# Performance work log

Measured on AMD Instinct MI355X. Metric: run time of the kernel, lower is better.

Reference implementation:

```python
import jax, jax.numpy as jnp
import numpy as np

N = 100000
E = 3200000


def setup_inputs() -> dict:
    key = jax.random.key(0)
    ks = jax.random.split(key, 8)
    x = jax.random.normal(ks[0], (N,), dtype=jnp.float32)
    edge_index = jax.random.randint(ks[1], (2, E), 0, N, dtype=jnp.int32)
    W_in = jax.random.normal(ks[2], (1, 32), dtype=jnp.float32) * 0.5
    b_in = jnp.zeros((32,), dtype=jnp.float32)
    W_mid = jax.random.normal(ks[3], (32, 32), dtype=jnp.float32) * (1.0 / np.sqrt(32))
    b_mid = jnp.zeros((32,), dtype=jnp.float32)
    W_out = jax.random.normal(ks[4], (32, 1), dtype=jnp.float32) * (1.0 / np.sqrt(32))
    b_out = jnp.zeros((1,), dtype=jnp.float32)
    return {"x": x, "edge_index": edge_index, "W_in": W_in, "b_in": b_in,
            "W_mid": W_mid, "b_mid": b_mid, "W_out": W_out, "b_out": b_out}


def _gcn_layer(h, src, dst, norm, W, b, n_nodes):
    # linear transform first (out_dim <= in_dim keeps message traffic small)
    h = h @ W                              # [N, out]
    msg = h[src] * norm[:, None]           # gather + edge-normalize, [E+N, out]
    out = jax.ops.segment_sum(msg, dst, num_segments=n_nodes)  # scatter-add
    return out + b


def reference(x, edge_index, W_in, b_in, W_mid, b_mid, W_out, b_out):
    n = x.shape[0]
    # add_self_loops
    loops = jnp.arange(n, dtype=edge_index.dtype)
    src = jnp.concatenate([edge_index[0], loops])
    dst = jnp.concatenate([edge_index[1], loops])
    # symmetric degree normalization (GCN): deg over target nodes incl. self loops
    deg = jax.ops.segment_sum(jnp.ones_like(src, dtype=x.dtype), dst, num_segments=n)
    dinv = jnp.where(deg > 0, jax.lax.rsqrt(deg), 0.0)
    norm = dinv[src] * dinv[dst]           # [E+N]

    h = x[:, None]                         # view(-1, 1)
    h = jax.nn.relu(_gcn_layer(h, src, dst, norm, W_in, b_in, n))
    h = jax.nn.relu(_gcn_layer(h, src, dst, norm, W_mid, b_mid, n))
    h = jax.nn.relu(_gcn_layer(h, src, dst, norm, W_mid, b_mid, n))  # conv_mid reused (shared weights)
    h = _gcn_layer(h, src, dst, norm, W_out, b_out, n)
    return jax.nn.sigmoid(h)               # [N, 1]
```

## Files before the change

### kernel.cpp

```cpp
#include <hip/hip_runtime.h>
#include <math.h>


#define BLK 256
#define PBLK 1024
#define BBLK 512
#define NBLK 256
#define MAXCHUNK 12544
#define BCAP 5120
#define SCAP 8448
#define SZCLAMP 5120

#define FP8_SCALE 64.0f
#define FP8_INV   0.015625f

typedef float f32x2 __attribute__((ext_vector_type(2)));


__global__ void k_initcur(int* __restrict__ cursor, int NB,
                          int* __restrict__ ph1, int* __restrict__ ph2) {
    int b = blockIdx.x * blockDim.x + threadIdx.x;
    if (b < NB) cursor[b] = b * BCAP;
    if (b < 8) { ph1[b] = 0; ph2[b] = 0; }
}

__global__ void __launch_bounds__(PBLK) k_place(
        const int* __restrict__ src, const int* __restrict__ dst,
        int* __restrict__ cursor, int* __restrict__ bkt, int E, int chunk) {
    __shared__ int hist[788];
    __shared__ int lofs[788];
    __shared__ int lcur[788];
    __shared__ int tmp[PBLK];
    __shared__ int stage[MAXCHUNK];
    int t = threadIdx.x;
    int b0 = blockIdx.x * chunk;
    int b1 = min(E, b0 + chunk);
    int n = b1 - b0;
    if (t < 788) hist[t] = 0;
    __syncthreads();
    for (int k = b0 + t; k < b1; k += PBLK) atomicAdd(&hist[dst[k] >> 7], 1);
    __syncthreads();
    int v = (t < 788) ? hist[t] : 0;
    tmp[t] = v;
    __syncthreads();
    for (int o = 1; o < PBLK; o <<= 1) {
        int a = (t >= o) ? tmp[t - o] : 0;
        __syncthreads();
        tmp[t] += a;
        __syncthreads();
    }
    int ex = tmp[t] - v;
    if (t < 788) { lofs[t] = ex; lcur[t] = ex; }
    __syncthreads();
    if (t < 782) {
        int c = hist[t];
        hist[t] = c ? atomicAdd(&cursor[t], c) : 0;
    }
    __syncthreads();
    for (int k = b0 + t; k < b1; k += PBLK) {
        int d = dst[k], s = src[k];
        int b = d >> 7;
        int p = atomicAdd(&lcur[b], 1);
        stage[p] = s | ((d & 127) << 17);
    }
    __syncthreads();
    for (int k = t; k < n; k += PBLK) {
        int lo = 0, hi = 781;
        while (lo < hi) {
            int mid = (lo + hi + 1) >> 1;
            if (lofs[mid] <= k) lo = mid; else hi = mid - 1;
        }
        int pos = hist[lo] + (k - lofs[lo]);
        if (pos < (lo + 1) * BCAP) bkt[pos] = stage[k];
    }
}

__global__ void __launch_bounds__(BBLK) k_build(
        const int* __restrict__ cursor, const int* __restrict__ bkt,
        const float* __restrict__ x,
        uint2* __restrict__ rs2, int* __restrict__ ss,
        float* __restrict__ dinv, float* __restrict__ sa, int N) {
    __shared__ int cnt[1024], lofs[1024], lcur[1024];
    __shared__ int tmp[BBLK];
    __shared__ int stg[SCAP];
    __shared__ int pB[128], pL[128];
    int b = blockIdx.x, t = threadIdx.x;
    int node_base = b << 7;
    int gb = b * BCAP;
    int gbs = b * SCAP;
    int sz = min(cursor[b] - gb, SZCLAMP);
    for (int i = t; i < 1024; i += BBLK) cnt[i] = 0;
    __syncthreads();
    const int* q = bkt + gb;
    for (int k = t; k < sz; k += BBLK) {
        int v = q[k];
        int bin = (((v >> 17) & 127) << 3) | ((v & 0x1FFFF) >> 14);
        atomicAdd(&cnt[bin], 1);
    }
    __syncthreads();
    int vals[2];
    int sum = 0;
    int i0 = t << 1;
    #pragma unroll
    for (int r = 0; r < 2; ++r) { vals[r] = cnt[i0 + r]; sum += vals[r]; }
    tmp[t] = sum;
    __syncthreads();
    for (int o = 1; o < BBLK; o <<= 1) {
        int a = (t >= o) ? tmp[t - o] : 0;
        __syncthreads();
        tmp[t] += a;
        __syncthreads();
    }
    int run = tmp[t] - sum;
    #pragma unroll
    for (int r = 0; r < 2; ++r) {
        int c = vals[r];
        lofs[i0 + r] = run;
        lcur[i0 + r] = run;
        run += c;
    }
    __syncthreads();
    int len = 0, padl = 0, real = 0;
    if (t < 128) {
        int i = node_base + t;
        if (i < N) {
            real = 1;
            int beg = lofs[t << 3];
            int end = (t < 127) ? lofs[(t + 1) << 3] : sz;
            len = end - beg;
            int deg = len + 1;
            padl = (deg + 7) & ~7;
            if (padl < 64) padl = 64;
        }
    }
    tmp[t] = (t < 128) ? padl : 0;
    __syncthreads();
    for (int o = 1; o < 128; o <<= 1) {
        int a = (t >= o && t < 128) ? tmp[t - o] : 0;
        __syncthreads();
        if (t < 128) tmp[t] += a;
        __syncthreads();
    }
    if (t < 128) {
        int pbeg = tmp[t] - padl;
        pB[t] = pbeg;
        pL[t] = real ? len : -1;
        if (real) {
            int i = node_base + t;
            int deg = len + 1;
            rs2[i] = make_uint2((unsigned)(gbs + pbeg), (unsigned)deg);
            float d = rsqrtf((float)deg);
            dinv[i] = d;
            sa[i] = x[i] * d;
        }
    }
    __syncthreads();
    int szp = min(tmp[127], SCAP);
    for (int i = t; i < 1024; i += BBLK) {
        int nn = i >> 3;
        lcur[i] = pB[nn] + (lofs[i] - lofs[nn << 3]);
    }
    __syncthreads();
    for (int k = t; k < sz; k += BBLK) {
        int v = q[k];
        int bin = (((v >> 17) & 127) << 3) | ((v & 0x1FFFF) >> 14);
        int pos = atomicAdd(&lcur[bin], 1);
        if (pos < SCAP) stg[pos] = (v & 0x1FFFF) << 5;
    }
    __syncthreads();
    if (t < 128 && pL[t] >= 0) {
        int pbeg = pB[t];
        int l2 = pL[t];
        int i = node_base + t;
        int deg = l2 + 1;
        int p2 = (deg + 7) & ~7;
        if (p2 < 64) p2 = 64;
        if (pbeg + l2 < SCAP) stg[pbeg + l2] = i << 5;
        for (int k = deg; k < p2; ++k)
            if (pbeg + k < SCAP) stg[pbeg + k] = N << 5;
    }
    __syncthreads();
    for (int k = t; k < szp; k += BBLK) ss[gbs + k] = stg[k];
}


__global__ void __launch_bounds__(BLK) k_l1aggG(
        const uint2* __restrict__ rs2, const int* __restrict__ ss,
        const float* __restrict__ sa, const float* __restrict__ dinv,
        const float* __restrict__ Win, const float* __restrict__ bin,
        const float* __restrict__ Wmid, unsigned char* __restrict__ Gh, int N) {
    __shared__ float sW[1024];
    int tid = threadIdx.x;
    #pragma unroll
    for (int r = 0; r < 4; ++r) sW[r * 256 + tid] = Wmid[r * 256 + tid];
    __syncthreads();
    int t = blockIdx.x * blockDim.x + tid;
    int i = t >> 5, l = t & 31;
    if (i >= N) return;
    uint2 r = rs2[i];
    int beg = (int)r.x, end = (int)(r.x + r.y);
    float s = 0.f;
    for (int e = beg + l; e < end; e += 32) s += sa[(unsigned)ss[e] >> 5];
    #pragma unroll
    for (int m = 16; m; m >>= 1) s += __shfl_xor(s, m, 32);
    float d = dinv[i];
    float h = d * s;
    float F = h * Win[l] + bin[l];
    F = F > 0.f ? F : 0.f;
    float g = 0.f;
    #pragma unroll
    for (int k = 0; k < 32; ++k) g += __shfl(F, k, 32) * sW[k * 32 + l];
    float v = g * d * FP8_SCALE;
    Gh[t] = (unsigned char)(__builtin_amdgcn_cvt_pk_fp8_f32(v, v, 0, false) & 0xFF);
}

__device__ __forceinline__ void acc_row(f32x2* a2, uint2 v) {
    a2[0] += __builtin_amdgcn_cvt_pk_f32_fp8(v.x, false);
    a2[1] += __builtin_amdgcn_cvt_pk_f32_fp8(v.x, true);
    a2[2] += __builtin_amdgcn_cvt_pk_f32_fp8(v.y, false);
    a2[3] += __builtin_amdgcn_cvt_pk_f32_fp8(v.y, true);
}

__device__ __forceinline__ void gather64(const unsigned char* __restrict__ Gb,
                                         const int* __restrict__ ss,
                                         int beg, int sub, int fo, int deg,
                                         f32x2* a2) {
    int sbeg = beg + sub;
    int idx[8];
    #pragma unroll
    for (int rr = 0; rr < 8; ++rr) idx[rr] = ss[sbeg + 8 * rr];
    uint2 v[8];
    #pragma unroll
    for (int rr = 0; rr < 8; ++rr)
        v[rr] = *(const uint2*)(Gb + (unsigned)(idx[rr] | fo));
    #pragma unroll
    for (int rr = 0; rr < 8; ++rr) acc_row(a2, v[rr]);
    int plen = (deg + 7) & ~7;
    plen = max(plen, 64);
    int wpl = max(plen, __shfl_xor(plen, 32));
    if (wpl > 64) {
        for (int so = 64 + sub; so < plen; so += 8) {
            int ix = ss[beg + so];
            uint2 vv = *(const uint2*)(Gb + (unsigned)(ix | fo));
            acc_row(a2, vv);
        }
    }
}

__device__ __forceinline__ void reduce_subs(f32x2* a2) {
    #pragma unroll
    for (int j = 0; j < 4; ++j) {
        #pragma unroll
        for (int m = 4; m <= 16; m <<= 1) {
            f32x2 o;
            o.x = __shfl_xor(a2[j].x, m);
            o.y = __shfl_xor(a2[j].y, m);
            a2[j] += o;
        }
    }
}

__global__ void __launch_bounds__(256) k_agg2mv(
        const uint2* __restrict__ rs2, const int* __restrict__ ss,
        const unsigned char* __restrict__ Gb, const float* __restrict__ dinv,
        const float* __restrict__ b, const float* __restrict__ Wmid,
        unsigned char* __restrict__ Gh3, int N) {
    __shared__ float sW2[1024];
    __shared__ float sF[8][34];
    __shared__ float sdv[8];
    int t = threadIdx.x;
    #pragma unroll
    for (int r = 0; r < 4; ++r) {
        int t4 = r * 256 + t;
        int k = t4 >> 5, ln = t4 & 31;
        sW2[(k >> 1) * 64 + ln * 2 + (k & 1)] = Wmid[t4];
    }
    int tg = blockIdx.x * blockDim.x + t;
    int g = tg >> 5;
    int lane = t & 31, sub = lane >> 2, fl = lane & 3;
    int grp = t >> 5;
    int fo = fl << 3;
    f32x2 a2[4];
    #pragma unroll
    for (int j = 0; j < 4; ++j) a2[j] = (f32x2)0.f;
    uint2 r = rs2[g];
    gather64(Gb, ss, (int)r.x, sub, fo, (int)r.y, a2);
    reduce_subs(a2);
    if (sub == 0) {
        float d = dinv[g];
        if (fl == 0) sdv[grp] = d;
        float ds = d * FP8_INV;
        #pragma unroll
        for (int j = 0; j < 8; ++j) {
            float v = ds * a2[j >> 1][j & 1] + b[fl * 8 + j];
            sF[grp][fl * 8 + j] = v > 0.f ? v : 0.f;
        }
    }
    __syncthreads();
    f32x2 s2 = (f32x2)0.f;
    #pragma unroll
    for (int k2 = 0; k2 < 16; ++k2) {
        f32x2 w2 = *(const f32x2*)&sW2[k2 * 64 + lane * 2];
        f32x2 f2 = *(const f32x2*)&sF[grp][k2 * 2];
        s2 += f2 * w2;
    }
    float s = s2.x + s2.y;
    float v = s * sdv[grp] * FP8_SCALE;
    Gh3[(long long)g * 32 + lane] =
        (unsigned char)(__builtin_amdgcn_cvt_pk_fp8_f32(v, v, 0, false) & 0xFF);
}

__global__ void __launch_bounds__(256) k_agg3(
        const uint2* __restrict__ rs2, const int* __restrict__ ss,
        const unsigned char* __restrict__ Gb, const float* __restrict__ dinv,
        const float* __restrict__ b, const float* __restrict__ Wout,
        float* __restrict__ sa, int N) {
    int t = blockIdx.x * blockDim.x + threadIdx.x;
    int g = t >> 5;
    if (g >= N) return;
    int lane = t & 31, sub = lane >> 2, fl = lane & 3;
    int fo = fl << 3;
    uint2 r = rs2[g];
    f32x2 a2[4];
    #pragma unroll
    for (int j = 0; j < 4; ++j) a2[j] = (f32x2)0.f;
    gather64(Gb, ss, (int)r.x, sub, fo, (int)r.y, a2);
    reduce_subs(a2);
    if (sub == 0) {
        float d = dinv[g];
        float ds = d * FP8_INV;
        float p = 0.f;
        #pragma unroll
        for (int j = 0; j < 8; ++j) {
            float v = ds * a2[j >> 1][j & 1] + b[fl * 8 + j];
            v = v > 0.f ? v : 0.f;
            p += v * Wout[fl * 8 + j];
        }
        p += __shfl_xor(p, 1, 32);
        p += __shfl_xor(p, 2, 32);
        if (fl == 0) sa[g] = p * d;
    }
}

__global__ void k_final_agg(const uint2* __restrict__ rs2, const int* __restrict__ ss,
                            const float* __restrict__ sa, const float* __restrict__ dinv,
                            const float* __restrict__ bout, float* __restrict__ out, int N) {
    int t = blockIdx.x * blockDim.x + threadIdx.x;
    int i = t >> 5, l = t & 31;
    if (i >= N) return;
    uint2 r = rs2[i];
    int beg = (int)r.x, end = (int)(r.x + r.y);
    float s = 0.f;
    for (int e = beg + l; e < end; e += 32) s += sa[(unsigned)ss[e] >> 5];
    #pragma unroll
    for (int m = 16; m; m >>= 1) s += __shfl_xor(s, m, 32);
    if (l == 0) {
        float z = dinv[i] * s + bout[0];
        out[i] = 1.0f / (1.0f + expf(-z));
    }
}

extern "C" void kernel_launch(void* const* d_in, const int* in_sizes, int n_in,
                              void* d_out, int out_size, void* d_ws, size_t ws_size,
                              hipStream_t stream) {
    const float* x    = (const float*)d_in[0];
    const int*   ei   = (const int*)  d_in[1];
    const float* Win  = (const float*)d_in[2];
    const float* bin  = (const float*)d_in[3];
    const float* Wmid = (const float*)d_in[4];
    const float* bmid = (const float*)d_in[5];
    const float* Wout = (const float*)d_in[6];
    const float* bout = (const float*)d_in[7];
    float* out = (float*)d_out;

    int N = in_sizes[0];
    int E = in_sizes[1] / 2;
    const int* src = ei;
    const int* dst = ei + E;

    int NB = (N + 127) >> 7;
    int chunk = (E + NBLK - 1) / NBLK;

    int* cursor = (int*)d_ws;
    uint2* rs2  = (uint2*)(cursor + 1024);
    int* ss     = (int*)(rs2 + N + 8);
    float* dinv = (float*)(ss + (size_t)NB * SCAP + 64);
    float* sa   = dinv + N;
    unsigned char* Gh  = (unsigned char*)(sa + N);
    unsigned char* Gh3 = Gh + 32 * (size_t)N + 32;
    int* bkt    = (int*)(Gh3 + 32 * (size_t)N + 32);

    int NT   = N * 32;
    int gN32 = (NT + BLK - 1) / BLK;

    k_initcur<<<(NB + BLK - 1) / BLK, BLK, 0, stream>>>(
        cursor, NB, (int*)(Gh + 32 * (size_t)N), (int*)(Gh3 + 32 * (size_t)N));
    k_place<<<NBLK, PBLK, 0, stream>>>(src, dst, cursor, bkt, E, chunk);
    k_build<<<NB, BBLK, 0, stream>>>(cursor, bkt, x, rs2, ss, dinv, sa, N);

    k_l1aggG<<<gN32, BLK, 0, stream>>>(rs2, ss, sa, dinv, Win, bin, Wmid, Gh, N);

    k_agg2mv<<<gN32, BLK, 0, stream>>>(rs2, ss, Gh, dinv, bmid, Wmid, Gh3, N);

    k_agg3<<<gN32, BLK, 0, stream>>>(rs2, ss, Gh3, dinv, bmid, Wout, sa, N);

    k_final_agg<<<gN32, BLK, 0, stream>>>(rs2, ss, sa, dinv, bout, out, N);
}
```

Measured before the change: 247.9 us.

## Process two nodes per wavefront-half in gather kernels and shrink per-node padding

Removes the minimum 64-slot padding per node in the CSR build, so the padded index list shrinks to degree rounded up to 8, and lowers the staging capacity to match. The layer-2 and layer-3 aggregation kernels now handle two destination nodes per 32-lane group, masking rows beyond each node's padded length to a phantom zero row. This gives more independent loads in flight per thread and halves the grid size. Layer 1's matvec is also rewritten to go through shared memory with paired float2 weights instead of 32 shuffles. The tradeoff is higher register pressure, and the smaller staging buffer could overflow for dense buckets.

```diff
diff --git a/kernel.cpp b/kernel.cpp
--- a/kernel.cpp
+++ b/kernel.cpp
@@ -8,7 +8,7 @@
 #define NBLK 256
 #define MAXCHUNK 12544
 #define BCAP 5120
-#define SCAP 8448
+#define SCAP 6144
 #define SZCLAMP 5120
 
 #define FP8_SCALE 64.0f
@@ -128,9 +128,7 @@
             int beg = lofs[t << 3];
             int end = (t < 127) ? lofs[(t + 1) << 3] : sz;
             len = end - beg;
-            int deg = len + 1;
-            padl = (deg + 7) & ~7;
-            if (padl < 64) padl = 64;
+            padl = (len + 8) & ~7;
         }
     }
     tmp[t] = (t < 128) ? padl : 0;
@@ -172,11 +170,9 @@
         int pbeg = pB[t];
         int l2 = pL[t];
         int i = node_base + t;
-        int deg = l2 + 1;
-        int p2 = (deg + 7) & ~7;
-        if (p2 < 64) p2 = 64;
+        int p2 = (l2 + 8) & ~7;
         if (pbeg + l2 < SCAP) stg[pbeg + l2] = i << 5;
-        for (int k = deg; k < p2; ++k)
+        for (int k = l2 + 1; k < p2; ++k)
             if (pbeg + k < SCAP) stg[pbeg + k] = N << 5;
     }
     __syncthreads();
@@ -189,29 +185,45 @@
         const float* __restrict__ sa, const float* __restrict__ dinv,
         const float* __restrict__ Win, const float* __restrict__ bin,
         const float* __restrict__ Wmid, unsigned char* __restrict__ Gh, int N) {
-    __shared__ float sW[1024];
+    __shared__ float sW2[1024];
+    __shared__ float sF[8][34];
     int tid = threadIdx.x;
     #pragma unroll
-    for (int r = 0; r < 4; ++r) sW[r * 256 + tid] = Wmid[r * 256 + tid];
+    for (int r = 0; r < 4; ++r) {
+        int t4 = r * 256 + tid;
+        int k = t4 >> 5, ln = t4 & 31;
+        sW2[(k >> 1) * 64 + ln * 2 + (k & 1)] = Wmid[t4];
+    }
     __syncthreads();
     int t = blockIdx.x * blockDim.x + tid;
     int i = t >> 5, l = t & 31;
-    if (i >= N) return;
-    uint2 r = rs2[i];
-    int beg = (int)r.x, end = (int)(r.x + r.y);
-    float s = 0.f;
-    for (int e = beg + l; e < end; e += 32) s += sa[(unsigned)ss[e] >> 5];
-    #pragma unroll
-    for (int m = 16; m; m >>= 1) s += __shfl_xor(s, m, 32);
-    float d = dinv[i];
-    float h = d * s;
-    float F = h * Win[l] + bin[l];
-    F = F > 0.f ? F : 0.f;
-    float g = 0.f;
-    #pragma unroll
-    for (int k = 0; k < 32; ++k) g += __shfl(F, k, 32) * sW[k * 32 + l];
-    float v = g * d * FP8_SCALE;
-    Gh[t] = (unsigned char)(__builtin_amdgcn_cvt_pk_fp8_f32(v, v, 0, false) & 0xFF);
+    int grp = tid >> 5;
+    bool act = (i < N);
+    float F = 0.f, d = 0.f;
+    if (act) {
+        uint2 r = rs2[i];
+        int beg = (int)r.x, end = (int)(r.x + r.y);
+        float s = 0.f;
+        for (int e = beg + l; e < end; e += 32) s += sa[(unsigned)ss[e] >> 5];
+        #pragma unroll
+        for (int m = 16; m; m >>= 1) s += __shfl_xor(s, m, 32);
+        d = dinv[i];
+        F = d * s * Win[l] + bin[l];
+        F = F > 0.f ? F : 0.f;
+    }
+    sF[grp][l] = F;
+    __syncthreads();
+    if (act) {
+        f32x2 s2 = (f32x2)0.f;
+        #pragma unroll
+        for (int k2 = 0; k2 < 16; ++k2) {
+            f32x2 w2 = *(const f32x2*)&sW2[k2 * 64 + l * 2];
+            f32x2 f2 = *(const f32x2*)&sF[grp][k2 * 2];
+            s2 += f2 * w2;
+        }
+        float v = (s2.x + s2.y) * d * FP8_SCALE;
+        Gh[t] = (unsigned char)(__builtin_amdgcn_cvt_pk_fp8_f32(v, v, 0, false) & 0xFF);
+    }
 }
 
 __device__ __forceinline__ void acc_row(f32x2* a2, uint2 v) {
@@ -221,29 +233,40 @@
     a2[3] += __builtin_amdgcn_cvt_pk_f32_fp8(v.y, true);
 }
 
-__device__ __forceinline__ void gather64(const unsigned char* __restrict__ Gb,
-                                         const int* __restrict__ ss,
-                                         int beg, int sub, int fo, int deg,
-                                         f32x2* a2) {
-    int sbeg = beg + sub;
-    int idx[8];
-    #pragma unroll
-    for (int rr = 0; rr < 8; ++rr) idx[rr] = ss[sbeg + 8 * rr];
-    uint2 v[8];
-    #pragma unroll
-    for (int rr = 0; rr < 8; ++rr)
-        v[rr] = *(const uint2*)(Gb + (unsigned)(idx[rr] | fo));
-    #pragma unroll
-    for (int rr = 0; rr < 8; ++rr) acc_row(a2, v[rr]);
-    int plen = (deg + 7) & ~7;
-    plen = max(plen, 64);
-    int wpl = max(plen, __shfl_xor(plen, 32));
-    if (wpl > 64) {
-        for (int so = 64 + sub; so < plen; so += 8) {
-            int ix = ss[beg + so];
-            uint2 vv = *(const uint2*)(Gb + (unsigned)(ix | fo));
-            acc_row(a2, vv);
-        }
+__device__ __forceinline__ void gather2(const unsigned char* __restrict__ Gb,
+                                        const int* __restrict__ ss,
+                                        int begA, int plenA, int begB, int plenB,
+                                        int sub, int fo, int phantom,
+                                        f32x2* aA, f32x2* aB) {
+    int sA = begA + sub, sB = begB + sub;
+    int iA[8], iB[8];
+    #pragma unroll
+    for (int r = 0; r < 8; ++r) iA[r] = ss[sA + 8 * r];
+    #pragma unroll
+    for (int r = 0; r < 8; ++r) iB[r] = ss[sB + 8 * r];
+    #pragma unroll
+    for (int r = 0; r < 8; ++r) {
+        iA[r] = (8 * r < plenA) ? iA[r] : phantom;
+        iB[r] = (8 * r < plenB) ? iB[r] : phantom;
+    }
+    uint2 vA[8], vB[8];
+    #pragma unroll
+    for (int r = 0; r < 8; ++r)
+        vA[r] = *(const uint2*)(Gb + (unsigned)(iA[r] | fo));
+    #pragma unroll
+    for (int r = 0; r < 8; ++r)
+        vB[r] = *(const uint2*)(Gb + (unsigned)(iB[r] | fo));
+    #pragma unroll
+    for (int r = 0; r < 8; ++r) acc_row(aA, vA[r]);
+    #pragma unroll
+    for (int r = 0; r < 8; ++r) acc_row(aB, vB[r]);
+    if (plenA > 64) {
+        for (int so = 64 + sub; so < plenA; so += 8)
+            acc_row(aA, *(const uint2*)(Gb + (unsigned)(ss[begA + so] | fo)));
+    }
+    if (plenB > 64) {
+        for (int so = 64 + sub; so < plenB; so += 8)
+            acc_row(aB, *(const uint2*)(Gb + (unsigned)(ss[begB + so] | fo)));
     }
 }
 
@@ -266,8 +289,8 @@
         const float* __restrict__ b, const float* __restrict__ Wmid,
         unsigned char* __restrict__ Gh3, int N) {
     __shared__ float sW2[1024];
-    __shared__ float sF[8][34];
-    __shared__ float sdv[8];
+    __shared__ float sF[8][2][34];
+    __shared__ float sdv[8][2];
     int t = threadIdx.x;
     #pragma unroll
     for (int r = 0; r < 4; ++r) {
@@ -275,39 +298,53 @@
         int k = t4 >> 5, ln = t4 & 31;
         sW2[(k >> 1) * 64 + ln * 2 + (k & 1)] = Wmid[t4];
     }
-    int tg = blockIdx.x * blockDim.x + t;
-    int g = tg >> 5;
+    int gid = (blockIdx.x * blockDim.x + t) >> 5;
+    int gA = gid * 2, gB = gA + 1;
     int lane = t & 31, sub = lane >> 2, fl = lane & 3;
     int grp = t >> 5;
     int fo = fl << 3;
-    f32x2 a2[4];
-    #pragma unroll
-    for (int j = 0; j < 4; ++j) a2[j] = (f32x2)0.f;
-    uint2 r = rs2[g];
-    gather64(Gb, ss, (int)r.x, sub, fo, (int)r.y, a2);
-    reduce_subs(a2);
+    int phantom = N << 5;
+    bool aAct = (gA < N), bAct = (gB < N);
+    uint2 rA = aAct ? rs2[gA] : make_uint2(0u, 0u);
+    uint2 rB = bAct ? rs2[gB] : make_uint2(0u, 0u);
+    int plenA = aAct ? (((int)rA.y + 7) & ~7) : 0;
+    int plenB = bAct ? (((int)rB.y + 7) & ~7) : 0;
+    f32x2 aA[4], aB[4];
+    #pragma unroll
+    for (int j = 0; j < 4; ++j) { aA[j] = (f32x2)0.f; aB[j] = (f32x2)0.f; }
+    gather2(Gb, ss, (int)rA.x, plenA, (int)rB.x, plenB, sub, fo, phantom, aA, aB);
+    reduce_subs(aA);
+    reduce_subs(aB);
     if (sub == 0) {
-        float d = dinv[g];
-        if (fl == 0) sdv[grp] = d;
-        float ds = d * FP8_INV;
+        float dA = aAct ? dinv[gA] : 0.f;
+        float dB = bAct ? dinv[gB] : 0.f;
+        if (fl == 0) { sdv[grp][0] = dA; sdv[grp][1] = dB; }
+        float dsA = dA * FP8_INV, dsB = dB * FP8_INV;
         #pragma unroll
         for (int j = 0; j < 8; ++j) {
-            float v = ds * a2[j >> 1][j & 1] + b[fl * 8 + j];
-            sF[grp][fl * 8 + j] = v > 0.f ? v : 0.f;
-        }
-    }
-    __syncthreads();
-    f32x2 s2 = (f32x2)0.f;
-    #pragma unroll
-    for (int k2 = 0; k2 < 16; ++k2) {
-        f32x2 w2 = *(const f32x2*)&sW2[k2 * 64 + lane * 2];
-        f32x2 f2 = *(const f32x2*)&sF[grp][k2 * 2];
-        s2 += f2 * w2;
-    }
-    float s = s2.x + s2.y;
-    float v = s * sdv[grp] * FP8_SCALE;
-    Gh3[(long long)g * 32 + lane] =
-        (unsigned char)(__builtin_amdgcn_cvt_pk_fp8_f32(v, v, 0, false) & 0xFF);
+            float bj = b[fl * 8 + j];
+            float vA = dsA * aA[j >> 1][j & 1] + bj;
+            float vB = dsB * aB[j >> 1][j & 1] + bj;
+            sF[grp][0][fl * 8 + j] = vA > 0.f ? vA : 0.f;
+            sF[grp][1][fl * 8 + j] = vB > 0.f ? vB : 0.f;
+        }
+    }
+    __syncthreads();
+    #pragma unroll
+    for (int n2 = 0; n2 < 2; ++n2) {
+        f32x2 s2 = (f32x2)0.f;
+        #pragma unroll
+        for (int k2 = 0; k2 < 16; ++k2) {
+            f32x2 w2 = *(const f32x2*)&sW2[k2 * 64 + lane * 2];
+            f32x2 f2 = *(const f32x2*)&sF[grp][n2][k2 * 2];
+            s2 += f2 * w2;
+        }
+        float v = (s2.x + s2.y) * sdv[grp][n2] * FP8_SCALE;
+        int g = gA + n2;
+        if (g < N)
+            Gh3[(long long)g * 32 + lane] =
+                (unsigned char)(__builtin_amdgcn_cvt_pk_fp8_f32(v, v, 0, false) & 0xFF);
+    }
 }
 
 __global__ void __launch_bounds__(256) k_agg3(
@@ -316,29 +353,45 @@
         const float* __restrict__ b, const float* __restrict__ Wout,
         float* __restrict__ sa, int N) {
     int t = blockIdx.x * blockDim.x + threadIdx.x;
-    int g = t >> 5;
-    if (g >= N) return;
+    int gid = t >> 5;
+    int gA = gid * 2, gB = gA + 1;
     int lane = t & 31, sub = lane >> 2, fl = lane & 3;
     int fo = fl << 3;
-    uint2 r = rs2[g];
-    f32x2 a2[4];
-    #pragma unroll
-    for (int j = 0; j < 4; ++j) a2[j] = (f32x2)0.f;
-    gather64(Gb, ss, (int)r.x, sub, fo, (int)r.y, a2);
-    reduce_subs(a2);
+    int phantom = N << 5;
+    bool aAct = (gA < N), bAct = (gB < N);
+    if (!aAct) return;
+    uint2 rA = rs2[gA];
+    uint2 rB = bAct ? rs2[gB] : make_uint2(0u, 0u);
+    int plenA = (((int)rA.y + 7) & ~7);
+    int plenB = bAct ? (((int)rB.y + 7) & ~7) : 0;
+    f32x2 aA[4], aB[4];
+    #pragma unroll
+    for (int j = 0; j < 4; ++j) { aA[j] = (f32x2)0.f; aB[j] = (f32x2)0.f; }
+    gather2(Gb, ss, (int)rA.x, plenA, (int)rB.x, plenB, sub, fo, phantom, aA, aB);
+    reduce_subs(aA);
+    reduce_subs(aB);
     if (sub == 0) {
-        float d = dinv[g];
-        float ds = d * FP8_INV;
-        float p = 0.f;
+        float dA = dinv[gA];
+        float dB = bAct ? dinv[gB] : 0.f;
+        float dsA = dA * FP8_INV, dsB = dB * FP8_INV;
+        float pA = 0.f, pB = 0.f;
         #pragma unroll
         for (int j = 0; j < 8; ++j) {
-            float v = ds * a2[j >> 1][j & 1] + b[fl * 8 + j];
-            v = v > 0.f ? v : 0.f;
-            p += v * Wout[fl * 8 + j];
-        }
-        p += __shfl_xor(p, 1, 32);
-        p += __shfl_xor(p, 2, 32);
-        if (fl == 0) sa[g] = p * d;
+            float bj = b[fl * 8 + j];
+            float wj = Wout[fl * 8 + j];
+            float vA = dsA * aA[j >> 1][j & 1] + bj;
+            float vB = dsB * aB[j >> 1][j & 1] + bj;
+            vA = vA > 0.f ? vA : 0.f;
+            vB = vB > 0.f ? vB : 0.f;
+            pA += vA * wj;
+            pB += vB * wj;
+        }
+        pA += __shfl_xor(pA, 1, 32); pA += __shfl_xor(pA, 2, 32);
+        pB += __shfl_xor(pB, 1, 32); pB += __shfl_xor(pB, 2, 32);
+        if (fl == 0) {
+            sa[gA] = pA * dA;
+            if (bAct) sa[gB] = pB * dB;
+        }
     }
 }
 
@@ -392,6 +445,7 @@
 
     int NT   = N * 32;
     int gN32 = (NT + BLK - 1) / BLK;
+    int gN16 = (N * 16 + BLK - 1) / BLK;
 
     k_initcur<<<(NB + BLK - 1) / BLK, BLK, 0, stream>>>(
         cursor, NB, (int*)(Gh + 32 * (size_t)N), (int*)(Gh3 + 32 * (size_t)N));
@@ -400,9 +454,9 @@
 
     k_l1aggG<<<gN32, BLK, 0, stream>>>(rs2, ss, sa, dinv, Win, bin, Wmid, Gh, N);
 
-    k_agg2mv<<<gN32, BLK, 0, stream>>>(rs2, ss, Gh, dinv, bmid, Wmid, Gh3, N);
-
-    k_agg3<<<gN32, BLK, 0, stream>>>(rs2, ss, Gh3, dinv, bmid, Wout, sa, N);
+    k_agg2mv<<<gN16, BLK, 0, stream>>>(rs2, ss, Gh, dinv, bmid, Wmid, Gh3, N);
+
+    k_agg3<<<gN16, BLK, 0, stream>>>(rs2, ss, Gh3, dinv, bmid, Wout, sa, N);
 
     k_final_agg<<<gN32, BLK, 0, stream>>>(rs2, ss, sa, dinv, bout, out, N);
 }
```

Measured after the change: 220.7 us. 1.12x faster.
